# Kernel tuning notes

Measured on AMD Instinct MI355X. Metric: run time of the kernel, lower is better.

Reference implementation:

```python
import jax, jax.numpy as jnp
import numpy as np

EPS = 1e-6

def ln(x):
    m = jnp.mean(x, axis=-1, keepdims=True)
    v = jnp.var(x, axis=-1, keepdims=True)
    return (x - m) * jax.lax.rsqrt(v + EPS)

def modulate(x, shift, scale):
    return x * (1.0 + scale[:, None, :]) + shift[:, None, :]

def setup_inputs() -> dict:
    key = jax.random.key(0)
    ks = jax.random.split(key, 16)
    B, N, H = 2, 384, 256
    D = 128  # n_vector_features * scale_dist_features
    MIN = 2 * H + D  # 640
    FH = 1024  # swiglu_correction_fn(4.0, 256)
    s = 0.02
    inp = {
        "mask": jnp.ones((B, N), jnp.float32),
        "x": jax.random.normal(ks[0], (B, N, H), jnp.float32),
        "t_emb": jax.random.normal(ks[1], (B, H), jnp.float32),
        "dist": jax.random.normal(ks[2], (B, N, N, D), jnp.float32),
        "edge_mask": jnp.ones((B, N, N), jnp.float32),
        "W_ada": jax.random.normal(ks[3], (6 * H, H), jnp.float32) * s,
        "b_ada": jnp.zeros((6 * H,), jnp.float32),
        "W_fe1": jax.random.normal(ks[4], (H, MIN), jnp.float32) * s,
        "b_fe1": jnp.zeros((H,), jnp.float32),
        "W_fe2": jax.random.normal(ks[5], (H, H), jnp.float32) * s,
        "b_fe2": jnp.zeros((H,), jnp.float32),
        "W_qkv": jax.random.normal(ks[6], (3 * H, H), jnp.float32) * s,
        "W_out": jax.random.normal(ks[7], (H, H), jnp.float32) * s,
        "W_ffn1": jax.random.normal(ks[8], (2 * FH, H), jnp.float32) * s,
        "W_ffn2": jax.random.normal(ks[9], (H, FH), jnp.float32) * s,
    }
    return inp

def reference(mask, x, t_emb, dist, edge_mask, W_ada, b_ada, W_fe1, b_fe1,
              W_fe2, b_fe2, W_qkv, W_out, W_ffn1, W_ffn2):
    B, N, H = x.shape
    num_heads = 8
    d_head = H // num_heads
    mN = mask[..., None]  # (B,N,1)

    # adaLN modulation
    ada = jax.nn.silu(t_emb) @ W_ada.T + b_ada  # (B,6H)
    shift_msa, scale_msa, gate_msa, shift_mlp, scale_mlp, gate_mlp = jnp.split(ada, 6, axis=1)

    x_norm = modulate(ln(x * mN), shift_msa, scale_msa)  # (B,N,H)

    # all-pairs message passing: concat(h_i, h_j, dist_ij) -> MLP -> sum_j
    h1 = jnp.broadcast_to(x_norm[:, :, None, :], (B, N, N, H))
    h2 = jnp.broadcast_to(x_norm[:, None, :, :], (B, N, N, H))
    feats = jnp.concatenate([h1, h2, dist], axis=-1) * edge_mask[..., None]
    msgs = jax.nn.silu(feats @ W_fe1.T + b_fe1) @ W_fe2.T + b_fe2  # (B,N,N,H)
    x_msg = jnp.sum(msgs, axis=-2)  # (B,N,H)

    # attention
    qkv = x_msg @ W_qkv.T
    Q, K, V = jnp.split(qkv, 3, axis=-1)
    Q = ln(Q * mN)
    K = ln(K * mN)
    def heads(t):
        return t.reshape(B, N, num_heads, d_head).transpose(0, 2, 1, 3)  # b h s d
    Q, K, V = heads(Q), heads(K), heads(V)
    scores = jnp.einsum("bhqd,bhkd->bhqk", Q, K) / jnp.sqrt(jnp.float32(d_head))
    bias = jnp.where(mask[:, None, None, :] > 0, 0.0, -1e9)
    attn = jax.nn.softmax(scores + bias, axis=-1)
    ao = jnp.einsum("bhqk,bhkd->bhqd", attn, V)
    ao = ao.transpose(0, 2, 1, 3).reshape(B, N, H)
    y = ao @ W_out.T

    x = x + gate_msa[:, None, :] * y

    # SwiGLU FFN
    xm = modulate(ln(x * mN), shift_mlp, scale_mlp)
    h12 = xm @ W_ffn1.T
    h_a, h_b = jnp.split(h12, 2, axis=-1)
    ffn_out = (jax.nn.silu(h_a) * h_b) @ W_ffn2.T
    x = (x + gate_mlp[:, None, :] * ffn_out) * mN
    return x
```

## Files before the change

kernel.cpp:

```cpp
#include <hip/hip_runtime.h>

#define DEVI __device__ __forceinline__

typedef float fv4 __attribute__((ext_vector_type(4)));
typedef __bf16 bf16x8 __attribute__((ext_vector_type(8)));
typedef unsigned short u16x8 __attribute__((ext_vector_type(8)));
typedef unsigned short u16x4 __attribute__((ext_vector_type(4)));

DEVI fv4 ldv4(const float* p) { return *reinterpret_cast<const fv4*>(p); }
DEVI bf16x8 pkbf(fv4 a, fv4 b) {
  bf16x8 r;
  r[0] = (__bf16)a[0]; r[1] = (__bf16)a[1]; r[2] = (__bf16)a[2]; r[3] = (__bf16)a[3];
  r[4] = (__bf16)b[0]; r[5] = (__bf16)b[1]; r[6] = (__bf16)b[2]; r[7] = (__bf16)b[3];
  return r;
}
DEVI u16x8 b2u(bf16x8 v) { return __builtin_bit_cast(u16x8, v); }
DEVI bf16x8 asbf(u16x8 u) { return __builtin_bit_cast(bf16x8, u); }
DEVI unsigned short bfbits(float x) { __bf16 v = (__bf16)x; return __builtin_bit_cast(unsigned short, v); }
DEVI u16x4 pk4(fv4 a) {
  u16x4 u;
  u[0] = bfbits(a[0]); u[1] = bfbits(a[1]); u[2] = bfbits(a[2]); u[3] = bfbits(a[3]);
  return u;
}
DEVI fv4 MFMA16(bf16x8 a, bf16x8 b, fv4 c) {
  return __builtin_amdgcn_mfma_f32_16x16x32_bf16(a, b, c, 0, 0, 0);
}
DEVI float siluf(float x) {
  float e = __builtin_amdgcn_exp2f(x * -1.44269504f);
  return x * __builtin_amdgcn_rcpf(1.f + e);
}
DEVI fv4 glu4(fv4 x, fv4 y) {
  fv4 r;
#pragma unroll
  for (int j = 0; j < 4; ++j) r[j] = siluf(x[j]) * y[j];
  return r;
}
DEVI int swz(int row, int k) {
  int unit = k >> 3;
  int phys = (unit & ~7) | ((unit ^ row) & 7);
  return row * 384 + (phys << 3) + (k & 7);
}

__global__ __launch_bounds__(256)
void k_ada(const float* __restrict__ temb, const float* __restrict__ W_ada,
           const float* __restrict__ b_ada, float* __restrict__ ada) {
  __shared__ float sm[256];
  const int b = blockIdx.x / 6;
  const int r = (blockIdx.x % 6) * 256 + threadIdx.x;
  sm[threadIdx.x] = siluf(temb[b * 256 + threadIdx.x]);
  __syncthreads();
  float s = b_ada[r];
  const float* wr = W_ada + (size_t)r * 256;
  for (int k = 0; k < 256; ++k) s += sm[k] * wr[k];
  ada[b * 1536 + r] = s;
}

__global__ __launch_bounds__(256)
void k_xnorm(const float* __restrict__ xin, const float* __restrict__ mask,
             const float* __restrict__ ada, int shift_off, int scale_off,
             float* __restrict__ out) {
  const int row = blockIdx.x;
  const int b = row / 384;
  const int t = threadIdx.x;
  const float m = mask[row];
  const float v = xin[(size_t)row * 256 + t] * m;
  float s = v, ss = v * v;
#pragma unroll
  for (int o = 1; o < 64; o <<= 1) { s += __shfl_xor(s, o); ss += __shfl_xor(ss, o); }
  __shared__ float red[8];
  const int wid = t >> 6;
  if ((t & 63) == 0) { red[wid] = s; red[4 + wid] = ss; }
  __syncthreads();
  s = red[0] + red[1] + red[2] + red[3];
  ss = red[4] + red[5] + red[6] + red[7];
  const float mean = s * (1.f / 256.f);
  const float var = ss * (1.f / 256.f) - mean * mean;
  const float rs = rsqrtf(var + 1e-6f);
  out[(size_t)row * 256 + t] =
      (v - mean) * rs * (1.f + ada[b * 1536 + scale_off + t]) + ada[b * 1536 + shift_off + t];
}

template <int EPI, int AMODE>
__global__ __launch_bounds__(256)
void k_gemm(const float* __restrict__ A, int lda,
            const float* __restrict__ B, int ldb, int koff, int K,
            float* __restrict__ C, int ldc,
            const float* __restrict__ bias, float bscale,
            const float* __restrict__ res,
            const float* __restrict__ ada, int gate_off,
            const float* __restrict__ mask) {
  __shared__ __align__(16) unsigned short As[64 * 64];
  __shared__ __align__(16) unsigned short Bs[64 * 64];
  const int t = threadIdx.x, lane = t & 63, w = t >> 6;
  const int bn0 = blockIdx.x * 64, bm0 = blockIdx.y * 64;
  const int qr = (w >> 1) * 32, qc = (w & 1) * 32;
  const int g = lane >> 4, c = lane & 15;
  const int srow = t >> 2;
  const int so = (t & 3) * 2;
  const int o0 = so ^ (srow & 7), o1 = (so + 1) ^ (srow & 7);
  unsigned short* aw0 = As + srow * 64 + o0 * 8;
  unsigned short* aw1 = As + srow * 64 + o1 * 8;
  unsigned short* bw0 = Bs + srow * 64 + o0 * 8;
  unsigned short* bw1 = Bs + srow * 64 + o1 * 8;
  const float* ag = A + (size_t)(bm0 + srow) * lda + so * 8;
  const float* bg = B + (size_t)(bn0 + srow) * ldb + koff + so * 8;
  const float* a2g = nullptr;
  if constexpr (AMODE == 2) a2g = res + ((size_t)(bm0 + srow) * lda + so * 8);
  fv4 a0 = ldv4(ag), a1 = ldv4(ag + 4), a2 = ldv4(ag + 8), a3 = ldv4(ag + 12);
  fv4 x0, x1, x2, x3;
  if constexpr (AMODE == 1) {
    x0 = ldv4(ag + 1024); x1 = ldv4(ag + 1028); x2 = ldv4(ag + 1032); x3 = ldv4(ag + 1036);
  }
  if constexpr (AMODE == 2) {
    x0 = ldv4(a2g); x1 = ldv4(a2g + 4); x2 = ldv4(a2g + 8); x3 = ldv4(a2g + 12);
  }
  fv4 c0 = ldv4(bg), c1 = ldv4(bg + 4), c2 = ldv4(bg + 8), c3 = ldv4(bg + 12);
  fv4 acc[2][2] = {};
  for (int k0 = 0; k0 < K; k0 += 64) {
    __syncthreads();
    if constexpr (AMODE == 1) {
      *reinterpret_cast<u16x8*>(aw0) = b2u(pkbf(glu4(a0, x0), glu4(a1, x1)));
      *reinterpret_cast<u16x8*>(aw1) = b2u(pkbf(glu4(a2, x2), glu4(a3, x3)));
    } else if constexpr (AMODE == 2) {
      *reinterpret_cast<u16x8*>(aw0) = b2u(pkbf(a0 + x0, a1 + x1));
      *reinterpret_cast<u16x8*>(aw1) = b2u(pkbf(a2 + x2, a3 + x3));
    } else {
      *reinterpret_cast<u16x8*>(aw0) = b2u(pkbf(a0, a1));
      *reinterpret_cast<u16x8*>(aw1) = b2u(pkbf(a2, a3));
    }
    *reinterpret_cast<u16x8*>(bw0) = b2u(pkbf(c0, c1));
    *reinterpret_cast<u16x8*>(bw1) = b2u(pkbf(c2, c3));
    __syncthreads();
    if (k0 + 64 < K) {
      ag += 64; bg += 64;
      a0 = ldv4(ag); a1 = ldv4(ag + 4); a2 = ldv4(ag + 8); a3 = ldv4(ag + 12);
      if constexpr (AMODE == 1) {
        x0 = ldv4(ag + 1024); x1 = ldv4(ag + 1028); x2 = ldv4(ag + 1032); x3 = ldv4(ag + 1036);
      }
      if constexpr (AMODE == 2) {
        a2g += 64;
        x0 = ldv4(a2g); x1 = ldv4(a2g + 4); x2 = ldv4(a2g + 8); x3 = ldv4(a2g + 12);
      }
      c0 = ldv4(bg); c1 = ldv4(bg + 4); c2 = ldv4(bg + 8); c3 = ldv4(bg + 12);
    }
#pragma unroll
    for (int kk = 0; kk < 2; ++kk) {
      bf16x8 af[2], bf[2];
#pragma unroll
      for (int mi = 0; mi < 2; ++mi) {
        int row = qr + mi * 16 + c;
        int oct = (kk * 4 + g) ^ (row & 7);
        af[mi] = asbf(*reinterpret_cast<const u16x8*>(As + row * 64 + oct * 8));
      }
#pragma unroll
      for (int ni = 0; ni < 2; ++ni) {
        int row = qc + ni * 16 + c;
        int oct = (kk * 4 + g) ^ (row & 7);
        bf[ni] = asbf(*reinterpret_cast<const u16x8*>(Bs + row * 64 + oct * 8));
      }
#pragma unroll
      for (int mi = 0; mi < 2; ++mi)
#pragma unroll
        for (int ni = 0; ni < 2; ++ni)
          acc[mi][ni] = MFMA16(af[mi], bf[ni], acc[mi][ni]);
    }
  }
#pragma unroll
  for (int mi = 0; mi < 2; ++mi)
#pragma unroll
    for (int ni = 0; ni < 2; ++ni)
#pragma unroll
      for (int r = 0; r < 4; ++r) {
        int row = bm0 + qr + mi * 16 + g * 4 + r;
        int col = bn0 + qc + ni * 16 + c;
        float v = acc[mi][ni][r];
        if constexpr (EPI == 1) v += bscale * bias[col];
        if constexpr (EPI == 2) v = res[(size_t)row * 256 + col] + ada[(row / 384) * 1536 + gate_off + col] * v;
        if constexpr (EPI == 3) v = (res[(size_t)row * 256 + col] + ada[(row / 384) * 1536 + gate_off + col] * v) * mask[row];
        if constexpr (EPI == 5) C[(((size_t)(row >> 4) * 256 + col) << 4) + (row & 15)] = v;
        else C[(size_t)row * ldc + col] = v;
      }
}

__global__ __launch_bounds__(256)
void k_edge(const float* __restrict__ dist, const float* __restrict__ emask,
            const float* __restrict__ Wfe1, const float* __restrict__ bfe1,
            const float* __restrict__ P, const float* __restrict__ Qc,
            float* __restrict__ S0, float* __restrict__ S1) {
  const int blk = blockIdx.x;
  const int jh = blockIdx.y;
  const int b = blk / 384, i = blk - b * 384;
  const int t = threadIdx.x, lane = t & 63, w = t >> 6;
  const int g = lane >> 4, c = lane & 15;
  const int l5 = lane >> 5, l31 = lane & 31;
  __shared__ __align__(16) unsigned short Al[2][4][16 * 136];

  bf16x8 Bf[4][4];
#pragma unroll
  for (int ht = 0; ht < 4; ++ht) {
    const int h = w * 64 + ht * 16 + c;
    const float* wp = Wfe1 + (size_t)h * 640 + 512 + g * 8;
#pragma unroll
    for (int ks = 0; ks < 4; ++ks)
      Bf[ht][ks] = pkbf(ldv4(wp + ks * 32), ldv4(wp + ks * 32 + 4));
  }
  float Pl[4], bl[4];
#pragma unroll
  for (int ht = 0; ht < 4; ++ht) {
    int h = w * 64 + ht * 16 + c;
    Pl[ht] = P[(size_t)(b * 384 + i) * 256 + h];
    bl[ht] = bfe1[h];
  }
  float Ss[4] = {0.f, 0.f, 0.f, 0.f};

  const float* dbase = dist + (size_t)(b * 384 + i) * 49152 + (size_t)jh * 24576;
  const float* embase = emask + (size_t)(b * 384 + i) * 384 + jh * 192;

  fv4 dreg[8];
#pragma unroll
  for (int tt = 0; tt < 8; ++tt) dreg[tt] = ldv4(dbase + tt * 256 + lane * 4);
#pragma unroll
  for (int tt = 0; tt < 8; ++tt) {
    int row = tt * 2 + l5;
    *reinterpret_cast<u16x4*>(&Al[0][w][row * 136 + l31 * 4]) = pk4(dreg[tt]);
  }
  for (int cl = 0; cl < 12; ++cl) {
    if (cl < 11) {
      const float* dg = dbase + (size_t)(cl + 1) * 2048 + lane * 4;
#pragma unroll
      for (int tt = 0; tt < 8; ++tt) dreg[tt] = ldv4(dg + tt * 256);
    }
    fv4 emv = ldv4(embase + cl * 16 + g * 4);
    const int jc = b * 24 + jh * 12 + cl;
    fv4 acc[4];
#pragma unroll
    for (int ht = 0; ht < 4; ++ht) {
      int h = w * 64 + ht * 16 + c;
      fv4 qv = ldv4(Qc + (((size_t)jc * 256 + h) << 4) + g * 4);
#pragma unroll
      for (int r = 0; r < 4; ++r) acc[ht][r] = Pl[ht] + qv[r];
    }
    const unsigned short* rb = &Al[cl & 1][w][0];
#pragma unroll
    for (int ks = 0; ks < 4; ++ks) {
      bf16x8 af = asbf(*reinterpret_cast<const u16x8*>(rb + c * 136 + ks * 32 + g * 8));
#pragma unroll
      for (int ht = 0; ht < 4; ++ht)
        acc[ht] = MFMA16(af, Bf[ht][ks], acc[ht]);
    }
#pragma unroll
    for (int ht = 0; ht < 4; ++ht)
#pragma unroll
      for (int r = 0; r < 4; ++r)
        Ss[ht] += siluf(emv[r] * acc[ht][r] + bl[ht]);
    if (cl < 11) {
      unsigned short* wb = &Al[(cl + 1) & 1][w][0];
#pragma unroll
      for (int tt = 0; tt < 8; ++tt) {
        int row = tt * 2 + l5;
        *reinterpret_cast<u16x4*>(&wb[row * 136 + l31 * 4]) = pk4(dreg[tt]);
      }
    }
  }
  float* Sp = jh ? S1 : S0;
#pragma unroll
  for (int ht = 0; ht < 4; ++ht) {
    float s = Ss[ht];
    s += __shfl_xor(s, 16);
    s += __shfl_xor(s, 32);
    if (g == 0) Sp[(size_t)(b * 384 + i) * 256 + w * 64 + ht * 16 + c] = s;
  }
}

__global__ __launch_bounds__(256)
void k_lnqk(const float* __restrict__ qkv, const float* __restrict__ mask,
            float* __restrict__ Qn, float* __restrict__ Kn) {
  const int row = blockIdx.x, t = threadIdx.x;
  const float m = mask[row];
  const float q = qkv[(size_t)row * 768 + t] * m;
  const float k = qkv[(size_t)row * 768 + 256 + t] * m;
  float sq = q, sqq = q * q, sk = k, skk = k * k;
#pragma unroll
  for (int o = 1; o < 64; o <<= 1) {
    sq += __shfl_xor(sq, o); sqq += __shfl_xor(sqq, o);
    sk += __shfl_xor(sk, o); skk += __shfl_xor(skk, o);
  }
  __shared__ float red[16];
  const int wid = t >> 6;
  if ((t & 63) == 0) { red[wid] = sq; red[4 + wid] = sqq; red[8 + wid] = sk; red[12 + wid] = skk; }
  __syncthreads();
  sq = red[0] + red[1] + red[2] + red[3];
  sqq = red[4] + red[5] + red[6] + red[7];
  sk = red[8] + red[9] + red[10] + red[11];
  skk = red[12] + red[13] + red[14] + red[15];
  const float mq = sq * (1.f / 256.f), vq = sqq * (1.f / 256.f) - mq * mq;
  const float mk = sk * (1.f / 256.f), vk = skk * (1.f / 256.f) - mk * mk;
  Qn[(size_t)row * 256 + t] = (q - mq) * rsqrtf(vq + 1e-6f);
  Kn[(size_t)row * 256 + t] = (k - mk) * rsqrtf(vk + 1e-6f);
}

__global__ __launch_bounds__(256)
void k_attn(const float* __restrict__ Qn, const float* __restrict__ Kn,
            const float* __restrict__ qkv, const float* __restrict__ mask,
            float* __restrict__ ao) {
  const int bh = blockIdx.y, b = bh >> 3, h = bh & 7;
  const int qg = blockIdx.x;
  const int t = threadIdx.x, lane = t & 63, w = t >> 6;
  const int g = lane >> 4, c = lane & 15;
  __shared__ __align__(16) unsigned short Vt[32 * 384];
  __shared__ __align__(16) unsigned short pl[16 * 384];
  __shared__ float outp[4][16][32];
  __shared__ float redm[4][16], reds[4][16];

  {
    const int d0 = (t & 7) * 4;
    const int kp = t >> 3;
#pragma unroll
    for (int pass = 0; pass < 6; ++pass) {
      int k = pass * 64 + kp * 2;
      fv4 v0 = ldv4(qkv + (size_t)(b * 384 + k) * 768 + 512 + h * 32 + d0);
      fv4 v1 = ldv4(qkv + (size_t)(b * 384 + k + 1) * 768 + 512 + h * 32 + d0);
#pragma unroll
      for (int j = 0; j < 4; ++j) {
        int d = d0 + j;
        unsigned int pr = (unsigned int)bfbits(v0[j]) | ((unsigned int)bfbits(v1[j]) << 16);
        *reinterpret_cast<unsigned int*>(&Vt[swz(d, k)]) = pr;
      }
    }
  }
  bf16x8 qf;
  {
    const float* qp = Qn + (size_t)(b * 384 + qg * 16 + c) * 256 + h * 32 + g * 8;
    qf = pkbf(ldv4(qp), ldv4(qp + 4));
  }
  fv4 sc[6];
#pragma unroll
  for (int kb = 0; kb < 6; ++kb) {
    const float* kp2 = Kn + (size_t)(b * 384 + w * 96 + kb * 16 + c) * 256 + h * 32 + g * 8;
    bf16x8 kf = pkbf(ldv4(kp2), ldv4(kp2 + 4));
    fv4 z = {0.f, 0.f, 0.f, 0.f};
    sc[kb] = MFMA16(qf, kf, z);
  }
  const float rs = 0.1767766952966369f;
  float zz[6][4], mx[4] = {-3e38f, -3e38f, -3e38f, -3e38f};
#pragma unroll
  for (int kb = 0; kb < 6; ++kb) {
    float mb = mask[b * 384 + w * 96 + kb * 16 + c] > 0.f ? 0.f : -1e9f;
#pragma unroll
    for (int r = 0; r < 4; ++r) {
      zz[kb][r] = sc[kb][r] * rs + mb;
      mx[r] = fmaxf(mx[r], zz[kb][r]);
    }
  }
#pragma unroll
  for (int r = 0; r < 4; ++r) {
#pragma unroll
    for (int o = 1; o < 16; o <<= 1) mx[r] = fmaxf(mx[r], __shfl_xor(mx[r], o));
  }
  if (c == 0) {
#pragma unroll
    for (int r = 0; r < 4; ++r) redm[w][g * 4 + r] = mx[r];
  }
  __syncthreads();
  float m4[4], sm[4] = {0.f, 0.f, 0.f, 0.f};
#pragma unroll
  for (int r = 0; r < 4; ++r) {
    int q = g * 4 + r;
    m4[r] = fmaxf(fmaxf(redm[0][q], redm[1][q]), fmaxf(redm[2][q], redm[3][q]));
  }
#pragma unroll
  for (int kb = 0; kb < 6; ++kb) {
    int k = w * 96 + kb * 16 + c;
#pragma unroll
    for (int r = 0; r < 4; ++r) {
      float p = __builtin_amdgcn_exp2f((zz[kb][r] - m4[r]) * 1.44269504f);
      sm[r] += p;
      pl[swz(g * 4 + r, k)] = bfbits(p);
    }
  }
#pragma unroll
  for (int r = 0; r < 4; ++r) {
#pragma unroll
    for (int o = 1; o < 16; o <<= 1) sm[r] += __shfl_xor(sm[r], o);
  }
  if (c == 0) {
#pragma unroll
    for (int r = 0; r < 4; ++r) reds[w][g * 4 + r] = sm[r];
  }
  __syncthreads();
  fv4 oacc[2] = {};
#pragma unroll
  for (int kk = 0; kk < 3; ++kk) {
    int kbase = w * 96 + kk * 32 + g * 8;
    bf16x8 pa = asbf(*reinterpret_cast<const u16x8*>(&pl[swz(c, kbase)]));
#pragma unroll
    for (int db = 0; db < 2; ++db) {
      int d = db * 16 + c;
      bf16x8 vb = asbf(*reinterpret_cast<const u16x8*>(&Vt[swz(d, kbase)]));
      oacc[db] = MFMA16(pa, vb, oacc[db]);
    }
  }
#pragma unroll
  for (int db = 0; db < 2; ++db)
#pragma unroll
    for (int r = 0; r < 4; ++r) outp[w][g * 4 + r][db * 16 + c] = oacc[db][r];
  __syncthreads();
#pragma unroll
  for (int idx = t; idx < 512; idx += 256) {
    int q = idx >> 5, d = idx & 31;
    float v = outp[0][q][d] + outp[1][q][d] + outp[2][q][d] + outp[3][q][d];
    float s = reds[0][q] + reds[1][q] + reds[2][q] + reds[3][q];
    ao[(size_t)(b * 384 + qg * 16 + q) * 256 + h * 32 + d] = v / s;
  }
}

extern "C" void kernel_launch(void* const* d_in, const int* in_sizes, int n_in,
                              void* d_out, int out_size, void* d_ws, size_t ws_size,
                              hipStream_t stream) {
  (void)in_sizes; (void)n_in; (void)out_size; (void)ws_size;
  const float* mask   = (const float*)d_in[0];
  const float* x      = (const float*)d_in[1];
  const float* temb   = (const float*)d_in[2];
  const float* dist   = (const float*)d_in[3];
  const float* emask  = (const float*)d_in[4];
  const float* W_ada  = (const float*)d_in[5];
  const float* b_ada  = (const float*)d_in[6];
  const float* W_fe1  = (const float*)d_in[7];
  const float* b_fe1  = (const float*)d_in[8];
  const float* W_fe2  = (const float*)d_in[9];
  const float* b_fe2  = (const float*)d_in[10];
  const float* W_qkv  = (const float*)d_in[11];
  const float* W_out  = (const float*)d_in[12];
  const float* W_ffn1 = (const float*)d_in[13];
  const float* W_ffn2 = (const float*)d_in[14];
  float* out = (float*)d_out;
  float* ws = (float*)d_ws;

  float* ada   = ws;
  float* xattn = ws + 4096;
  float* xm    = ws + 200704;
  float* xn    = ws + 397312;
  float* P     = ws + 593920;
  float* Qc    = ws + 790528;
  float* S0    = ws + 987136;
  float* xmsg  = ws + 1183744;
  float* qkvb  = ws + 1380352;
  float* Qn    = ws + 1970176;
  float* Kn    = ws + 2166784;
  float* aob   = ws + 2363392;
  float* S1    = ws + 2363392;
  float* h12   = ws + 397312;

  k_ada<<<12, 256, 0, stream>>>(temb, W_ada, b_ada, ada);
  k_xnorm<<<768, 256, 0, stream>>>(x, mask, ada, 0, 256, xn);
  k_gemm<0, 0><<<dim3(4, 12), 256, 0, stream>>>(xn, 256, W_fe1, 640, 0, 256, P, 256,
                                                nullptr, 0.f, nullptr, nullptr, 0, nullptr);
  k_gemm<5, 0><<<dim3(4, 12), 256, 0, stream>>>(xn, 256, W_fe1, 640, 256, 256, Qc, 0,
                                                nullptr, 0.f, nullptr, nullptr, 0, nullptr);
  k_edge<<<dim3(768, 2), 256, 0, stream>>>(dist, emask, W_fe1, b_fe1, P, Qc, S0, S1);
  k_gemm<1, 2><<<dim3(4, 12), 256, 0, stream>>>(S0, 256, W_fe2, 256, 0, 256, xmsg, 256,
                                                b_fe2, 384.f, S1, nullptr, 0, nullptr);
  k_gemm<0, 0><<<dim3(12, 12), 256, 0, stream>>>(xmsg, 256, W_qkv, 256, 0, 256, qkvb, 768,
                                                 nullptr, 0.f, nullptr, nullptr, 0, nullptr);
  k_lnqk<<<768, 256, 0, stream>>>(qkvb, mask, Qn, Kn);
  k_attn<<<dim3(24, 16), 256, 0, stream>>>(Qn, Kn, qkvb, mask, aob);
  k_gemm<2, 0><<<dim3(4, 12), 256, 0, stream>>>(aob, 256, W_out, 256, 0, 256, xattn, 256,
                                                nullptr, 0.f, x, ada, 512, nullptr);
  k_xnorm<<<768, 256, 0, stream>>>(xattn, mask, ada, 768, 1024, xm);
  k_gemm<0, 0><<<dim3(32, 12), 256, 0, stream>>>(xm, 256, W_ffn1, 256, 0, 256, h12, 2048,
                                                 nullptr, 0.f, nullptr, nullptr, 0, nullptr);
  k_gemm<3, 1><<<dim3(4, 12), 256, 0, stream>>>(h12, 2048, W_ffn2, 1024, 0, 1024, out, 256,
                                                nullptr, 0.f, xattn, ada, 1280, mask);
}
```

Before: 170.1 us.

## Share dist tile across waves in k_edge with swizzled LDS and prefetch

Before, each of the four waves loaded and converted its own full copy of every 16x128 dist chunk, so the block read the same chunk four times. Now all 256 threads cooperatively load one chunk into a single shared, XOR-swizzled LDS buffer, which cuts the redundant global traffic and the register pressure from the old 8-vector per-lane prefetch. The edge-mask and Qc values for the next chunk are also prefetched into registers one iteration ahead. In exchange, a block-wide barrier is added every iteration and the loop is no longer unrolled.

```diff
diff --git a/kernel.cpp b/kernel.cpp
--- a/kernel.cpp
+++ b/kernel.cpp
@@ -187,15 +187,14 @@
             const float* __restrict__ Wfe1, const float* __restrict__ bfe1,
             const float* __restrict__ P, const float* __restrict__ Qc,
             float* __restrict__ S0, float* __restrict__ S1) {
-  const int blk = blockIdx.x;
-  const int jh = blockIdx.y;
+  const int blk = blockIdx.x, jh = blockIdx.y;
   const int b = blk / 384, i = blk - b * 384;
   const int t = threadIdx.x, lane = t & 63, w = t >> 6;
   const int g = lane >> 4, c = lane & 15;
-  const int l5 = lane >> 5, l31 = lane & 31;
-  __shared__ __align__(16) unsigned short Al[2][4][16 * 136];
+  __shared__ __align__(16) unsigned short Al[2][16 * 128];
 
   bf16x8 Bf[4][4];
+  float Pl[4], bl[4], Ss[4] = {0.f, 0.f, 0.f, 0.f};
 #pragma unroll
   for (int ht = 0; ht < 4; ++ht) {
     const int h = w * 64 + ht * 16 + c;
@@ -203,50 +202,58 @@
 #pragma unroll
     for (int ks = 0; ks < 4; ++ks)
       Bf[ht][ks] = pkbf(ldv4(wp + ks * 32), ldv4(wp + ks * 32 + 4));
-  }
-  float Pl[4], bl[4];
-#pragma unroll
-  for (int ht = 0; ht < 4; ++ht) {
-    int h = w * 64 + ht * 16 + c;
     Pl[ht] = P[(size_t)(b * 384 + i) * 256 + h];
     bl[ht] = bfe1[h];
   }
-  float Ss[4] = {0.f, 0.f, 0.f, 0.f};
-
   const float* dbase = dist + (size_t)(b * 384 + i) * 49152 + (size_t)jh * 24576;
   const float* embase = emask + (size_t)(b * 384 + i) * 384 + jh * 192;
-
-  fv4 dreg[8];
-#pragma unroll
-  for (int tt = 0; tt < 8; ++tt) dreg[tt] = ldv4(dbase + tt * 256 + lane * 4);
-#pragma unroll
-  for (int tt = 0; tt < 8; ++tt) {
-    int row = tt * 2 + l5;
-    *reinterpret_cast<u16x4*>(&Al[0][w][row * 136 + l31 * 4]) = pk4(dreg[tt]);
-  }
+  const int jcb = b * 24 + jh * 12;
+
+  const int srow = t >> 4, sunit = t & 15;
+  const int sphys = (sunit & 8) | ((sunit ^ (srow & 7)) & 7);
+  const int soff = srow * 128 + sphys * 8;
+  const float* sg = dbase + srow * 128 + sunit * 8;
+
+  {
+    fv4 d0 = ldv4(sg), d1 = ldv4(sg + 4);
+    *reinterpret_cast<u16x8*>(&Al[0][soff]) = b2u(pkbf(d0, d1));
+  }
+  fv4 emv = ldv4(embase + g * 4);
+  fv4 qv[4];
+#pragma unroll
+  for (int ht = 0; ht < 4; ++ht)
+    qv[ht] = ldv4(Qc + (((size_t)jcb * 256 + w * 64 + ht * 16 + c) << 4) + g * 4);
+  __syncthreads();
+
+#pragma unroll 1
   for (int cl = 0; cl < 12; ++cl) {
+    fv4 p0, p1;
     if (cl < 11) {
-      const float* dg = dbase + (size_t)(cl + 1) * 2048 + lane * 4;
-#pragma unroll
-      for (int tt = 0; tt < 8; ++tt) dreg[tt] = ldv4(dg + tt * 256);
-    }
-    fv4 emv = ldv4(embase + cl * 16 + g * 4);
-    const int jc = b * 24 + jh * 12 + cl;
+      const float* pg = sg + (size_t)(cl + 1) * 2048;
+      p0 = ldv4(pg); p1 = ldv4(pg + 4);
+    }
     fv4 acc[4];
 #pragma unroll
     for (int ht = 0; ht < 4; ++ht) {
-      int h = w * 64 + ht * 16 + c;
-      fv4 qv = ldv4(Qc + (((size_t)jc * 256 + h) << 4) + g * 4);
-#pragma unroll
-      for (int r = 0; r < 4; ++r) acc[ht][r] = Pl[ht] + qv[r];
-    }
-    const unsigned short* rb = &Al[cl & 1][w][0];
+#pragma unroll
+      for (int r = 0; r < 4; ++r) acc[ht][r] = Pl[ht] + qv[ht][r];
+    }
+    const unsigned short* rb = &Al[cl & 1][0];
 #pragma unroll
     for (int ks = 0; ks < 4; ++ks) {
-      bf16x8 af = asbf(*reinterpret_cast<const u16x8*>(rb + c * 136 + ks * 32 + g * 8));
+      const int u = ks * 4 + g;
+      const int phys = (u & 8) | ((u ^ (c & 7)) & 7);
+      bf16x8 af = asbf(*reinterpret_cast<const u16x8*>(rb + c * 128 + phys * 8));
+#pragma unroll
+      for (int ht = 0; ht < 4; ++ht) acc[ht] = MFMA16(af, Bf[ht][ks], acc[ht]);
+    }
+    fv4 emn, qn[4];
+    if (cl < 11) {
+      emn = ldv4(embase + (cl + 1) * 16 + g * 4);
+      const size_t jc = (size_t)(jcb + cl + 1);
 #pragma unroll
       for (int ht = 0; ht < 4; ++ht)
-        acc[ht] = MFMA16(af, Bf[ht][ks], acc[ht]);
+        qn[ht] = ldv4(Qc + ((jc * 256 + w * 64 + ht * 16 + c) << 4) + g * 4);
     }
 #pragma unroll
     for (int ht = 0; ht < 4; ++ht)
@@ -254,13 +261,12 @@
       for (int r = 0; r < 4; ++r)
         Ss[ht] += siluf(emv[r] * acc[ht][r] + bl[ht]);
     if (cl < 11) {
-      unsigned short* wb = &Al[(cl + 1) & 1][w][0];
-#pragma unroll
-      for (int tt = 0; tt < 8; ++tt) {
-        int row = tt * 2 + l5;
-        *reinterpret_cast<u16x4*>(&wb[row * 136 + l31 * 4]) = pk4(dreg[tt]);
-      }
-    }
+      *reinterpret_cast<u16x8*>(&Al[(cl + 1) & 1][soff]) = b2u(pkbf(p0, p1));
+      emv = emn;
+#pragma unroll
+      for (int ht = 0; ht < 4; ++ht) qv[ht] = qn[ht];
+    }
+    __syncthreads();
   }
   float* Sp = jh ? S1 : S0;
 #pragma unroll
```

New measurement: 163.0 us. -4.2%, faster.
